# Performance work log

Hardware: AMD Instinct MI355X
Metric: run time of the kernel (lower is better)

Reference implementation:

```python
import jax, jax.numpy as jnp
import numpy as np

HIDDEN = 4096
N_HEADS = 32
N_KV = 32
HEAD_DIM = HIDDEN // N_HEADS  # 128
T = 2048
THETA = 10000.0
EPS = 1e-5


def setup_inputs() -> dict:
    key = jax.random.key(0)
    ks = jax.random.split(key, 7)
    s = 0.02
    return {
        "positions": jnp.arange(T, dtype=jnp.int64),
        "hidden_states": jax.random.normal(ks[0], (T, HIDDEN), jnp.float32),
        "w_qkv": jax.random.normal(ks[1], ((N_HEADS + 2 * N_KV) * HEAD_DIM, HIDDEN), jnp.float32) * s,
        "w_o": jax.random.normal(ks[2], (HIDDEN, N_HEADS * HEAD_DIM), jnp.float32) * s,
        "q_norm_w": jnp.ones((N_HEADS, HEAD_DIM), jnp.float32) + jax.random.normal(ks[3], (N_HEADS, HEAD_DIM), jnp.float32) * s,
        "q_norm_b": jax.random.normal(ks[4], (N_HEADS, HEAD_DIM), jnp.float32) * s,
        "k_norm_w": jnp.ones((N_KV, HEAD_DIM), jnp.float32) + jax.random.normal(ks[5], (N_KV, HEAD_DIM), jnp.float32) * s,
        "k_norm_b": jax.random.normal(ks[6], (N_KV, HEAD_DIM), jnp.float32) * s,
    }


def _layer_norm_affine(x, w, b):
    # x: [T, H, d]; normalize over last dim, no affine inside, then per-head affine
    mu = jnp.mean(x, axis=-1, keepdims=True)
    var = jnp.var(x, axis=-1, keepdims=True)
    xn = (x - mu) * jax.lax.rsqrt(var + EPS)
    return xn * w + b


def _rope_neox(x, positions):
    # x: [T, H, d], NEOX style: rotate halves over full head_dim
    half = HEAD_DIM // 2
    inv_freq = 1.0 / (THETA ** (jnp.arange(0, half, dtype=jnp.float32) * 2.0 / HEAD_DIM))
    ang = positions.astype(jnp.float32)[:, None] * inv_freq  # [T, half]
    cos = jnp.cos(ang)[:, None, :]
    sin = jnp.sin(ang)[:, None, :]
    x1, x2 = x[..., :half], x[..., half:]
    return jnp.concatenate([x1 * cos - x2 * sin, x2 * cos + x1 * sin], axis=-1)


def reference(positions, hidden_states, w_qkv, w_o, q_norm_w, q_norm_b, k_norm_w, k_norm_b):
    qkv = hidden_states @ w_qkv.T  # [T, (H+2Hkv)*d]
    q_size = N_HEADS * HEAD_DIM
    kv_size = N_KV * HEAD_DIM
    q = qkv[:, :q_size].reshape(T, N_HEADS, HEAD_DIM)
    k = qkv[:, q_size:q_size + kv_size].reshape(T, N_KV, HEAD_DIM)
    v = qkv[:, q_size + kv_size:].reshape(T, N_KV, HEAD_DIM)

    q = _layer_norm_affine(q, q_norm_w, q_norm_b)
    k = _layer_norm_affine(k, k_norm_w, k_norm_b)
    q = _rope_neox(q, positions)
    k = _rope_neox(k, positions)

    scale = HEAD_DIM ** -0.5
    scores = jnp.einsum('thd,shd->hts', q, k) * scale  # [H, T, T]
    causal = jnp.tril(jnp.ones((T, T), dtype=bool))
    scores = jnp.where(causal[None], scores, jnp.finfo(scores.dtype).min)
    p = jax.nn.softmax(scores, axis=-1)
    attn = jnp.einsum('hts,shd->thd', p, v).reshape(T, N_HEADS * HEAD_DIM)
    return attn @ w_o.T
```

## Files before the change

### kernel.cpp

```cpp
#include <hip/hip_runtime.h>
#include <cstdint>

#define T_SEQ 2048
#define HID   4096
#define NH    32
#define HD    128
#define QKVW  12288

typedef float  f32x4  __attribute__((ext_vector_type(4)));
typedef __bf16 bf16x8 __attribute__((ext_vector_type(8)));

#define QSCALE (0.08838834764831845f * 1.4426950408889634f)

__device__ __forceinline__ unsigned short f2bf(float f) {
  unsigned int u = __builtin_bit_cast(unsigned int, f);
  u += 0x7fffu + ((u >> 16) & 1u);
  return (unsigned short)(u >> 16);
}

__device__ __forceinline__ void gload_lds16(const void* gptr, void* lptr) {
  __builtin_amdgcn_global_load_lds(
      (const __attribute__((address_space(1))) unsigned int*)(unsigned long long)(uintptr_t)gptr,
      (__attribute__((address_space(3))) unsigned int*)(unsigned int)(uintptr_t)lptr,
      16, 0, 0);
}

#define SB __builtin_amdgcn_sched_barrier(0)

__global__ __launch_bounds__(256) void cast_bf16(const float* __restrict__ in,
                                                 unsigned short* __restrict__ out,
                                                 int n4) {
  int i = blockIdx.x * 256 + threadIdx.x;
  int stride = gridDim.x * 256;
  for (; i < n4; i += stride) {
    float4 v = ((const float4*)in)[i];
    ushort4 o;
    o.x = f2bf(v.x); o.y = f2bf(v.y); o.z = f2bf(v.z); o.w = f2bf(v.w);
    ((ushort4*)out)[i] = o;
  }
}

__global__ __launch_bounds__(512, 2) void gemm_bt(const unsigned short* __restrict__ Ag,
                                                  const unsigned short* __restrict__ Bg,
                                                  float* __restrict__ C,
                                                  int M, int N, int K, int MT) {
  __shared__ unsigned short As_[2][128 * 64];
  __shared__ unsigned short Bs_[2][256 * 64];
  const int tid  = threadIdx.x;
  const int lane = tid & 63;
  const int w    = tid >> 6;
  const int wm   = w >> 2;
  const int wn   = w & 3;
  const int l15  = lane & 15;
  const int lg   = lane >> 4;

  const int nwg = gridDim.x;
  const int cpx = nwg >> 3;
  const int swz = (blockIdx.x & 7) * cpx + (blockIdx.x >> 3);
  const int bm  = (swz % MT) * 128;
  const int bn  = (swz / MT) * 256;
  const int nk  = K >> 6;

#define STAGE_A(buf, kt_) do {                                                   \
    const unsigned short* _s = Ag + (size_t)bm * K + (size_t)(kt_) * 64;         \
    _Pragma("unroll")                                                            \
    for (int _u = 0; _u < 2; ++_u) {                                             \
      const int _cid = _u * 512 + tid;                                           \
      const int _r = _cid >> 3, _ch = _cid & 7;                                  \
      gload_lds16(_s + (size_t)_r * K + ((_ch ^ (_r & 7)) * 8),                  \
                  &As_[buf][(_u * 512 + w * 64) * 8]);                           \
    } } while (0)

#define STAGE_B(buf, kt_) do {                                                   \
    const unsigned short* _s = Bg + (size_t)bn * K + (size_t)(kt_) * 64;         \
    _Pragma("unroll")                                                            \
    for (int _u = 0; _u < 4; ++_u) {                                             \
      const int _cid = _u * 512 + tid;                                           \
      const int _r = _cid >> 3, _ch = _cid & 7;                                  \
      gload_lds16(_s + (size_t)_r * K + ((_ch ^ (_r & 7)) * 8),                  \
                  &Bs_[buf][(_u * 512 + w * 64) * 8]);                           \
    } } while (0)

  f32x4 acc[4][4] = {};

  STAGE_A(0, 0);
  STAGE_B(0, 0);
  if (nk > 1) {
    STAGE_B(1, 1);
    asm volatile("s_waitcnt vmcnt(4)" ::: "memory");
  } else {
    asm volatile("s_waitcnt vmcnt(0)" ::: "memory");
  }
  __builtin_amdgcn_s_barrier();

  for (int t = 0; t < nk; ++t) {
    const int cur = t & 1;
    bf16x8 bfr[4][2];
#pragma unroll
    for (int n = 0; n < 4; ++n)
#pragma unroll
      for (int kk = 0; kk < 2; ++kk) {
        const int r = wn * 64 + n * 16 + l15;
        bfr[n][kk] = *(const bf16x8*)&Bs_[cur][r * 64 + (((kk * 4 + lg) ^ (r & 7)) * 8)];
      }
    bf16x8 a0[2][2];
#pragma unroll
    for (int mi = 0; mi < 2; ++mi)
#pragma unroll
      for (int kk = 0; kk < 2; ++kk) {
        const int r = wm * 64 + mi * 16 + l15;
        a0[mi][kk] = *(const bf16x8*)&As_[cur][r * 64 + (((kk * 4 + lg) ^ (r & 7)) * 8)];
      }
    if (t + 1 < nk) STAGE_A(cur ^ 1, t + 1);
    __builtin_amdgcn_s_barrier();
    __builtin_amdgcn_s_setprio(1);
#pragma unroll
    for (int mi = 0; mi < 2; ++mi)
#pragma unroll
      for (int n = 0; n < 4; ++n)
#pragma unroll
        for (int kk = 0; kk < 2; ++kk)
          acc[mi][n] = __builtin_amdgcn_mfma_f32_16x16x32_bf16(a0[mi][kk], bfr[n][kk], acc[mi][n], 0, 0, 0);
    __builtin_amdgcn_s_setprio(0);
    __builtin_amdgcn_s_barrier();

    bf16x8 a1[2][2];
#pragma unroll
    for (int mi = 0; mi < 2; ++mi)
#pragma unroll
      for (int kk = 0; kk < 2; ++kk) {
        const int r = wm * 64 + (2 + mi) * 16 + l15;
        a1[mi][kk] = *(const bf16x8*)&As_[cur][r * 64 + (((kk * 4 + lg) ^ (r & 7)) * 8)];
      }
    if (t + 2 < nk) STAGE_B(cur, t + 2);
    __builtin_amdgcn_s_barrier();
    __builtin_amdgcn_s_setprio(1);
#pragma unroll
    for (int mi = 0; mi < 2; ++mi)
#pragma unroll
      for (int n = 0; n < 4; ++n)
#pragma unroll
        for (int kk = 0; kk < 2; ++kk)
          acc[2 + mi][n] = __builtin_amdgcn_mfma_f32_16x16x32_bf16(a1[mi][kk], bfr[n][kk], acc[2 + mi][n], 0, 0, 0);
    __builtin_amdgcn_s_setprio(0);
    if (t + 1 < nk) {
      if (t + 2 < nk) asm volatile("s_waitcnt vmcnt(4)" ::: "memory");
      else            asm volatile("s_waitcnt vmcnt(0)" ::: "memory");
      __builtin_amdgcn_sched_barrier(0);
    }
    __builtin_amdgcn_s_barrier();
  }
#undef STAGE_A
#undef STAGE_B

#pragma unroll
  for (int m = 0; m < 4; ++m)
#pragma unroll
    for (int i = 0; i < 4; ++i) {
      const int row = bm + wm * 64 + m * 16 + lg * 4 + i;
#pragma unroll
      for (int n = 0; n < 4; ++n)
        C[(size_t)row * N + bn + wn * 64 + n * 16 + l15] = acc[m][n][i];
    }
}

__global__ __launch_bounds__(512, 2) void gemm_bt8(const unsigned short* __restrict__ Ag,
                                                   const unsigned short* __restrict__ Bg,
                                                   float* __restrict__ C,
                                                   int M, int N, int K, int MT) {
  __shared__ unsigned short As_[2][256 * 64];
  __shared__ unsigned short Bs_[2][256 * 64];
  const int tid  = threadIdx.x;
  const int lane = tid & 63;
  const int w    = tid >> 6;
  const int wm   = w >> 2;
  const int wn   = w & 3;
  const int l15  = lane & 15;
  const int lg   = lane >> 4;
  const int sw   = l15 & 7;

  const int cpx = gridDim.x >> 3;
  const int swz = (blockIdx.x & 7) * cpx + (blockIdx.x >> 3);
  const int bm  = (swz % MT) * 256;
  const int bn  = (swz / MT) * 256;
  const int nk  = K >> 6;

  const unsigned short* Abase = Ag + (size_t)bm * K;
  const unsigned short* Bbase = Bg + (size_t)bn * K;

#define SG(ldsbase, gbase, kt_, u_) do {                                        \
    const int _cid = (u_) * 512 + tid;                                          \
    const int _r = _cid >> 3, _ch = _cid & 7;                                   \
    gload_lds16((gbase) + (size_t)_r * K + (size_t)(kt_) * 64 +                 \
                    ((_ch ^ (_r & 7)) * 8),                                     \
                (void*)((char*)(ldsbase) + _cid * 16));                         \
  } while (0)

#define RD(base, r, kk)                                                          \
  (*(const bf16x8*)((const char*)(base) + (r) * 128 + ((((kk) * 4 + lg) ^ sw) * 16)))

#define MFMA16(mbase, afr, bfr) do {                                             \
    _Pragma("unroll")                                                            \
    for (int _m = 0; _m < 4; ++_m)                                               \
      _Pragma("unroll")                                                          \
      for (int _n = 0; _n < 4; ++_n)                                             \
        acc[(mbase) + _m][_n] = __builtin_amdgcn_mfma_f32_16x16x32_bf16(         \
            afr[_m], bfr[_n], acc[(mbase) + _m][_n], 0, 0, 0);                   \
  } while (0)

  f32x4 acc[8][4] = {};

#pragma unroll
  for (int u = 0; u < 4; ++u) SG(As_[0], Abase, 0, u);
#pragma unroll
  for (int u = 0; u < 4; ++u) SG(Bs_[0], Bbase, 0, u);
  if (nk > 1) {
#pragma unroll
    for (int u = 0; u < 4; ++u) SG(As_[1], Abase, 1, u);
#pragma unroll
    for (int u = 0; u < 4; ++u) SG(Bs_[1], Bbase, 1, u);
    asm volatile("s_waitcnt vmcnt(8)" ::: "memory");
  } else {
    asm volatile("s_waitcnt vmcnt(0)" ::: "memory");
  }
  SB;
  __builtin_amdgcn_s_barrier();

  for (int t = 0; t < nk; ++t) {
    const int cur = t & 1;
    const unsigned short* As = As_[cur];
    const unsigned short* Bs = Bs_[cur];
    bf16x8 a0[4], a1[4], a2[4], a3[4], b0[4], b1[4];

#pragma unroll
    for (int m = 0; m < 4; ++m) a0[m] = RD(As, wm * 128 + m * 16 + l15, 0);
#pragma unroll
    for (int n = 0; n < 4; ++n) b0[n] = RD(Bs, wn * 64 + n * 16 + l15, 0);
    SB;
#pragma unroll
    for (int m = 0; m < 4; ++m) a1[m] = RD(As, wm * 128 + m * 16 + l15, 1);
#pragma unroll
    for (int n = 0; n < 4; ++n) b1[n] = RD(Bs, wn * 64 + n * 16 + l15, 1);
    SB;
    asm volatile("s_waitcnt lgkmcnt(8)" ::: "memory");
    SB;
    __builtin_amdgcn_s_setprio(1);
    MFMA16(0, a0, b0);
    __builtin_amdgcn_s_setprio(0);
#pragma unroll
    for (int m = 0; m < 4; ++m) a2[m] = RD(As, wm * 128 + (4 + m) * 16 + l15, 0);
    SB;
    asm volatile("s_waitcnt lgkmcnt(4)" ::: "memory");
    SB;
    __builtin_amdgcn_s_setprio(1);
    MFMA16(0, a1, b1);
    __builtin_amdgcn_s_setprio(0);
    __builtin_amdgcn_s_barrier();
#pragma unroll
    for (int m = 0; m < 4; ++m) a3[m] = RD(As, wm * 128 + (4 + m) * 16 + l15, 1);
    SB;
    if (t + 2 < nk) {
#pragma unroll
      for (int u = 0; u < 4; ++u) SG(As_[cur], Abase, t + 2, u);
#pragma unroll
      for (int u = 0; u < 4; ++u) SG(Bs_[cur], Bbase, t + 2, u);
    }
    SB;
    asm volatile("s_waitcnt lgkmcnt(4)" ::: "memory");
    SB;
    __builtin_amdgcn_s_setprio(1);
    MFMA16(4, a2, b0);
    __builtin_amdgcn_s_setprio(0);
    SB;
    asm volatile("s_waitcnt lgkmcnt(0)" ::: "memory");
    SB;
    __builtin_amdgcn_s_setprio(1);
    MFMA16(4, a3, b1);
    __builtin_amdgcn_s_setprio(0);
    if (t + 1 < nk) {
      if (t + 2 < nk) asm volatile("s_waitcnt vmcnt(8)" ::: "memory");
      else            asm volatile("s_waitcnt vmcnt(0)" ::: "memory");
      SB;
      __builtin_amdgcn_s_barrier();
    }
  }
#undef SG
#undef RD
#undef MFMA16

#pragma unroll
  for (int m = 0; m < 8; ++m)
#pragma unroll
    for (int i = 0; i < 4; ++i) {
      const int row = bm + wm * 128 + m * 16 + lg * 4 + i;
#pragma unroll
      for (int n = 0; n < 4; ++n)
        C[(size_t)row * N + bn + wn * 64 + n * 16 + l15] = acc[m][n][i];
    }
}

__global__ __launch_bounds__(256) void norm_rope(const float* __restrict__ qkv,
                                                 const float* __restrict__ qw,
                                                 const float* __restrict__ qb,
                                                 const float* __restrict__ kw,
                                                 const float* __restrict__ kb,
                                                 unsigned short* __restrict__ q,
                                                 unsigned short* __restrict__ k,
                                                 unsigned short* __restrict__ v) {
  const int t    = blockIdx.x;
  const int tid  = threadIdx.x;
  const int lane = tid & 63;
  const int w    = tid >> 6;
  const float invf = exp2f(-(float)lane * (13.287712379549449f / 64.0f));
  const float ang  = (float)t * invf;
  const float c = cosf(ang), s = sinf(ang);
  const float* row = qkv + (size_t)t * QKVW;

#pragma unroll 1
  for (int sel = 0; sel < 2; ++sel) {
    const float* src = row + sel * HID;
    const float* wgt = sel ? kw : qw;
    const float* bia = sel ? kb : qb;
    unsigned short* dst = sel ? k : q;
    const float oscale = sel ? 1.0f : QSCALE;
    for (int h = w; h < NH; h += 4) {
      const float* x = src + h * HD;
      float x1 = x[lane], x2 = x[lane + 64];
      float sum = x1 + x2, ss = x1 * x1 + x2 * x2;
#pragma unroll
      for (int m = 1; m < 64; m <<= 1) {
        sum += __shfl_xor(sum, m, 64);
        ss  += __shfl_xor(ss, m, 64);
      }
      const float mu  = sum * (1.0f / 128.0f);
      const float var = ss * (1.0f / 128.0f) - mu * mu;
      const float r   = rsqrtf(var + 1e-5f);
      const float n1  = (x1 - mu) * r * wgt[h * HD + lane]      + bia[h * HD + lane];
      const float n2  = (x2 - mu) * r * wgt[h * HD + lane + 64] + bia[h * HD + lane + 64];
      const float o1  = (n1 * c - n2 * s) * oscale;
      const float o2  = (n2 * c + n1 * s) * oscale;
      dst[(size_t)t * HID + h * HD + lane]      = f2bf(o1);
      dst[(size_t)t * HID + h * HD + lane + 64] = f2bf(o2);
    }
  }
  const float* vx = row + 2 * HID;
  unsigned short* vdst = v + (size_t)t * HID;
  for (int j = tid; j < HID / 4; j += 256) {
    float4 val = ((const float4*)vx)[j];
    ushort4 o;
    o.x = f2bf(val.x); o.y = f2bf(val.y); o.z = f2bf(val.z); o.w = f2bf(val.w);
    ((ushort4*)vdst)[j] = o;
  }
}

__global__ __launch_bounds__(256) void transpose_v(const unsigned short* __restrict__ v,
                                                   unsigned short* __restrict__ vt) {
  __shared__ unsigned short tile[64][65];
  const int h  = blockIdx.z;
  const int tt = blockIdx.x * 64;
  const int dd = blockIdx.y * 64;
  const int tid = threadIdx.x;
#pragma unroll
  for (int p = 0; p < 4; ++p) {
    int idx = p * 256 + tid;
    int r = idx >> 4, c4 = idx & 15;
    ushort4 val = *(const ushort4*)&v[(size_t)(tt + r) * HID + h * HD + dd + c4 * 4];
    tile[r][c4 * 4 + 0] = val.x;
    tile[r][c4 * 4 + 1] = val.y;
    tile[r][c4 * 4 + 2] = val.z;
    tile[r][c4 * 4 + 3] = val.w;
  }
  __syncthreads();
#pragma unroll
  for (int p = 0; p < 4; ++p) {
    int idx = p * 256 + tid;
    int r = idx >> 4, c4 = idx & 15;
    ushort4 o;
    o.x = tile[c4 * 4 + 0][r];
    o.y = tile[c4 * 4 + 1][r];
    o.z = tile[c4 * 4 + 2][r];
    o.w = tile[c4 * 4 + 3][r];
    *(ushort4*)&vt[((size_t)h * HD + dd + r) * T_SEQ + tt + c4 * 4] = o;
  }
}

__global__ __launch_bounds__(256) void attn_fwd(const unsigned short* __restrict__ Q,
                                                const unsigned short* __restrict__ K,
                                                const unsigned short* __restrict__ VT,
                                                unsigned short* __restrict__ O) {
  __shared__ unsigned short Ks[2][64 * 128];
  __shared__ unsigned short Vs[2][128 * 64];
  __shared__ unsigned short Ps[4][16 * 64];
  const int h    = blockIdx.y;
  const int pair = blockIdx.x;
  const int tid  = threadIdx.x;
  const int lane = tid & 63;
  const int w    = tid >> 6;
  const int l15  = lane & 15;
  const int lg   = lane >> 4;
  const int sw   = l15 & 7;

#pragma unroll 1
  for (int half = 0; half < 2; ++half) {
    const int qt   = half ? (31 - pair) : pair;
    const int qrow = qt * 64 + w * 16;

    bf16x8 qf[4];
#pragma unroll
    for (int kk = 0; kk < 4; ++kk)
      qf[kk] = *(const bf16x8*)&Q[(size_t)(qrow + l15) * HID + h * HD + kk * 32 + lg * 8];

    f32x4 o[8] = {};
    float mrow[4], lrow[4];
#pragma unroll
    for (int i = 0; i < 4; ++i) { mrow[i] = -1e30f; lrow[i] = 0.0f; }

    const int nkt = qt + 1;

    {
#pragma unroll
      for (int p = 0; p < 4; ++p) {
        const int c  = p * 256 + tid;
        const int kr = c >> 4, kc = c & 15;
        gload_lds16(&K[(size_t)kr * HID + h * HD + ((kc ^ (kr & 7)) * 8)],
                    &Ks[0][(p * 256 + w * 64) * 8]);
        const int vr = c >> 3, vc = c & 7;
        gload_lds16(&VT[((size_t)h * HD + vr) * T_SEQ + ((vc ^ (vr & 7)) * 8)],
                    &Vs[0][(p * 256 + w * 64) * 8]);
      }
    }
    __syncthreads();

#pragma unroll 1
    for (int kt = 0; kt < nkt; ++kt) {
      const int cur = kt & 1;
      if (kt + 1 < nkt) {
        const int k0 = (kt + 1) * 64;
#pragma unroll
        for (int p = 0; p < 4; ++p) {
          const int c  = p * 256 + tid;
          const int kr = c >> 4, kc = c & 15;
          gload_lds16(&K[(size_t)(k0 + kr) * HID + h * HD + ((kc ^ (kr & 7)) * 8)],
                      &Ks[cur ^ 1][(p * 256 + w * 64) * 8]);
          const int vr = c >> 3, vc = c & 7;
          gload_lds16(&VT[((size_t)h * HD + vr) * T_SEQ + k0 + ((vc ^ (vr & 7)) * 8)],
                      &Vs[cur ^ 1][(p * 256 + w * 64) * 8]);
        }
      }
      const unsigned short* ksb = Ks[cur];
      const unsigned short* vsb = Vs[cur];

      f32x4 sfr[4] = {};
#pragma unroll
      for (int n = 0; n < 4; ++n)
#pragma unroll
        for (int kk = 0; kk < 4; ++kk) {
          bf16x8 kf = *(const bf16x8*)&ksb[(n * 16 + l15) * 128 + ((kk * 4 + lg) ^ sw) * 8];
          sfr[n] = __builtin_amdgcn_mfma_f32_16x16x32_bf16(qf[kk], kf, sfr[n], 0, 0, 0);
        }

      if (kt == qt) {
#pragma unroll
        for (int n = 0; n < 4; ++n)
#pragma unroll
          for (int i = 0; i < 4; ++i)
            if (n * 16 + l15 > w * 16 + lg * 4 + i) sfr[n][i] = -1e30f;
      }

      float escale[4];
#pragma unroll
      for (int i = 0; i < 4; ++i) {
        float mx = fmaxf(fmaxf(sfr[0][i], sfr[1][i]), fmaxf(sfr[2][i], sfr[3][i]));
        mx = fmaxf(mx, __shfl_xor(mx, 1, 64));
        mx = fmaxf(mx, __shfl_xor(mx, 2, 64));
        mx = fmaxf(mx, __shfl_xor(mx, 4, 64));
        mx = fmaxf(mx, __shfl_xor(mx, 8, 64));
        const float mnew = fmaxf(mrow[i], mx);
        escale[i] = exp2f(mrow[i] - mnew);
        mrow[i] = mnew;
        const int prow = lg * 4 + i;
        float rs = 0.0f;
#pragma unroll
        for (int n = 0; n < 4; ++n) {
          const float p = exp2f(sfr[n][i] - mnew);
          rs += p;
          Ps[w][prow * 64 + (((2 * n + (l15 >> 3)) ^ (prow & 7)) * 8) + sw] = f2bf(p);
        }
        rs += __shfl_xor(rs, 1, 64);
        rs += __shfl_xor(rs, 2, 64);
        rs += __shfl_xor(rs, 4, 64);
        rs += __shfl_xor(rs, 8, 64);
        lrow[i] = lrow[i] * escale[i] + rs;
      }
#pragma unroll
      for (int f = 0; f < 8; ++f)
#pragma unroll
        for (int i = 0; i < 4; ++i) o[f][i] *= escale[i];

      asm volatile("s_waitcnt lgkmcnt(0)" ::: "memory");
      __builtin_amdgcn_sched_barrier(0);

      bf16x8 pf[2];
#pragma unroll
      for (int kk = 0; kk < 2; ++kk)
        pf[kk] = *(const bf16x8*)&Ps[w][l15 * 64 + ((kk * 4 + lg) ^ sw) * 8];
#pragma unroll
      for (int f = 0; f < 8; ++f)
#pragma unroll
        for (int kk = 0; kk < 2; ++kk) {
          bf16x8 vf = *(const bf16x8*)&vsb[(f * 16 + l15) * 64 + ((kk * 4 + lg) ^ sw) * 8];
          o[f] = __builtin_amdgcn_mfma_f32_16x16x32_bf16(pf[kk], vf, o[f], 0, 0, 0);
        }

      __syncthreads();
    }

#pragma unroll
    for (int i = 0; i < 4; ++i) {
      const float inv = 1.0f / lrow[i];
      const int trow = qrow + lg * 4 + i;
#pragma unroll
      for (int f = 0; f < 8; ++f)
        O[(size_t)trow * HID + h * HD + f * 16 + l15] = f2bf(o[f][i] * inv);
    }
  }
}

extern "C" void kernel_launch(void* const* d_in, const int* in_sizes, int n_in,
                              void* d_out, int out_size, void* d_ws, size_t ws_size,
                              hipStream_t stream) {
  const float* hidden = (const float*)d_in[1];
  const float* w_qkv  = (const float*)d_in[2];
  const float* w_o    = (const float*)d_in[3];
  const float* qw     = (const float*)d_in[4];
  const float* qb     = (const float*)d_in[5];
  const float* kw     = (const float*)d_in[6];
  const float* kb     = (const float*)d_in[7];

  char* ws = (char*)d_ws;
  unsigned short* wqkv_bf = (unsigned short*)(ws + 0);
  unsigned short* attn_bf = (unsigned short*)(ws + 0);
  unsigned short* wo_bf   = (unsigned short*)(ws + 16777216);
  unsigned short* hid_bf  = (unsigned short*)(ws + 100663296);
  unsigned short* vt_bf   = (unsigned short*)(ws + 100663296);
  float* qkv_f32          = (float*)(ws + 117440512);
  unsigned short* q_bf    = (unsigned short*)(ws + 218103808);
  unsigned short* k_bf    = (unsigned short*)(ws + 234881024);
  unsigned short* v_bf    = (unsigned short*)(ws + 251658240);

  cast_bf16<<<2048, 256, 0, stream>>>(hidden, hid_bf, (T_SEQ * HID) / 4);
  cast_bf16<<<2048, 256, 0, stream>>>(w_qkv, wqkv_bf, (QKVW * HID) / 4);
  gemm_bt8<<<384, 512, 0, stream>>>(hid_bf, wqkv_bf, qkv_f32, T_SEQ, QKVW, HID, 8);
  cast_bf16<<<2048, 256, 0, stream>>>(w_o, wo_bf, (HID * HID) / 4);
  norm_rope<<<T_SEQ, 256, 0, stream>>>(qkv_f32, qw, qb, kw, kb, q_bf, k_bf, v_bf);
  transpose_v<<<dim3(T_SEQ / 64, HD / 64, NH), 256, 0, stream>>>(v_bf, vt_bf);
  attn_fwd<<<dim3(16, NH), 256, 0, stream>>>(q_bf, k_bf, vt_bf, attn_bf);
  gemm_bt<<<256, 512, 0, stream>>>(attn_bf, wo_bf, (float*)d_out, T_SEQ, HID, HID, 16);
}
```

Baseline: 503.2 us.

## Emit bf16 QKV from GEMM, retile to 256x192, drop V cast pass

The QKV GEMM now writes bf16 output instead of fp32, which halves the intermediate write and read traffic. Its block tile moves from 256x256 to 256x192, giving a 512-block grid instead of 384 so the work spreads more evenly across CUs. norm_rope reads bf16 input and no longer copies V, and transpose_v reads V directly from the QKV buffer with stride QKVW. Rounding Q and K to bf16 before layer norm adds precision loss, and the narrower N tile lowers MFMA reuse per LDS load.

```diff
diff --git a/kernel.cpp b/kernel.cpp
--- a/kernel.cpp
+++ b/kernel.cpp
@@ -16,6 +16,9 @@
   unsigned int u = __builtin_bit_cast(unsigned int, f);
   u += 0x7fffu + ((u >> 16) & 1u);
   return (unsigned short)(u >> 16);
+}
+__device__ __forceinline__ float bf2f(unsigned short u) {
+  return __builtin_bit_cast(float, (unsigned int)u << 16);
 }
 
 __device__ __forceinline__ void gload_lds16(const void* gptr, void* lptr) {
@@ -166,10 +169,10 @@
 
 __global__ __launch_bounds__(512, 2) void gemm_bt8(const unsigned short* __restrict__ Ag,
                                                    const unsigned short* __restrict__ Bg,
-                                                   float* __restrict__ C,
+                                                   unsigned short* __restrict__ C,
                                                    int M, int N, int K, int MT) {
   __shared__ unsigned short As_[2][256 * 64];
-  __shared__ unsigned short Bs_[2][256 * 64];
+  __shared__ unsigned short Bs_[2][192 * 64];
   const int tid  = threadIdx.x;
   const int lane = tid & 63;
   const int w    = tid >> 6;
@@ -182,7 +185,7 @@
   const int cpx = gridDim.x >> 3;
   const int swz = (blockIdx.x & 7) * cpx + (blockIdx.x >> 3);
   const int bm  = (swz % MT) * 256;
-  const int bn  = (swz / MT) * 256;
+  const int bn  = (swz / MT) * 192;
   const int nk  = K >> 6;
 
   const unsigned short* Abase = Ag + (size_t)bm * K;
@@ -195,31 +198,31 @@
                     ((_ch ^ (_r & 7)) * 8),                                     \
                 (void*)((char*)(ldsbase) + _cid * 16));                         \
   } while (0)
+#define STAGE(abuf, bbuf, kt_) do {                                             \
+    SG(abuf, Abase, kt_, 0); SG(abuf, Abase, kt_, 1);                           \
+    SG(abuf, Abase, kt_, 2); SG(abuf, Abase, kt_, 3);                           \
+    SG(bbuf, Bbase, kt_, 0); SG(bbuf, Bbase, kt_, 1);                           \
+    SG(bbuf, Bbase, kt_, 2);                                                    \
+  } while (0)
 
 #define RD(base, r, kk)                                                          \
   (*(const bf16x8*)((const char*)(base) + (r) * 128 + ((((kk) * 4 + lg) ^ sw) * 16)))
 
-#define MFMA16(mbase, afr, bfr) do {                                             \
+#define MFMA12(mbase, afr, bfr) do {                                             \
     _Pragma("unroll")                                                            \
     for (int _m = 0; _m < 4; ++_m)                                               \
       _Pragma("unroll")                                                          \
-      for (int _n = 0; _n < 4; ++_n)                                             \
+      for (int _n = 0; _n < 3; ++_n)                                             \
         acc[(mbase) + _m][_n] = __builtin_amdgcn_mfma_f32_16x16x32_bf16(         \
             afr[_m], bfr[_n], acc[(mbase) + _m][_n], 0, 0, 0);                   \
   } while (0)
 
-  f32x4 acc[8][4] = {};
-
-#pragma unroll
-  for (int u = 0; u < 4; ++u) SG(As_[0], Abase, 0, u);
-#pragma unroll
-  for (int u = 0; u < 4; ++u) SG(Bs_[0], Bbase, 0, u);
+  f32x4 acc[8][3] = {};
+
+  STAGE(As_[0], Bs_[0], 0);
   if (nk > 1) {
-#pragma unroll
-    for (int u = 0; u < 4; ++u) SG(As_[1], Abase, 1, u);
-#pragma unroll
-    for (int u = 0; u < 4; ++u) SG(Bs_[1], Bbase, 1, u);
-    asm volatile("s_waitcnt vmcnt(8)" ::: "memory");
+    STAGE(As_[1], Bs_[1], 1);
+    asm volatile("s_waitcnt vmcnt(7)" ::: "memory");
   } else {
     asm volatile("s_waitcnt vmcnt(0)" ::: "memory");
   }
@@ -230,22 +233,22 @@
     const int cur = t & 1;
     const unsigned short* As = As_[cur];
     const unsigned short* Bs = Bs_[cur];
-    bf16x8 a0[4], a1[4], a2[4], a3[4], b0[4], b1[4];
+    bf16x8 a0[4], a1[4], a2[4], a3[4], b0[3], b1[3];
 
 #pragma unroll
     for (int m = 0; m < 4; ++m) a0[m] = RD(As, wm * 128 + m * 16 + l15, 0);
 #pragma unroll
-    for (int n = 0; n < 4; ++n) b0[n] = RD(Bs, wn * 64 + n * 16 + l15, 0);
+    for (int n = 0; n < 3; ++n) b0[n] = RD(Bs, wn * 48 + n * 16 + l15, 0);
     SB;
 #pragma unroll
     for (int m = 0; m < 4; ++m) a1[m] = RD(As, wm * 128 + m * 16 + l15, 1);
 #pragma unroll
-    for (int n = 0; n < 4; ++n) b1[n] = RD(Bs, wn * 64 + n * 16 + l15, 1);
-    SB;
-    asm volatile("s_waitcnt lgkmcnt(8)" ::: "memory");
+    for (int n = 0; n < 3; ++n) b1[n] = RD(Bs, wn * 48 + n * 16 + l15, 1);
+    SB;
+    asm volatile("s_waitcnt lgkmcnt(7)" ::: "memory");
     SB;
     __builtin_amdgcn_s_setprio(1);
-    MFMA16(0, a0, b0);
+    MFMA12(0, a0, b0);
     __builtin_amdgcn_s_setprio(0);
 #pragma unroll
     for (int m = 0; m < 4; ++m) a2[m] = RD(As, wm * 128 + (4 + m) * 16 + l15, 0);
@@ -253,40 +256,36 @@
     asm volatile("s_waitcnt lgkmcnt(4)" ::: "memory");
     SB;
     __builtin_amdgcn_s_setprio(1);
-    MFMA16(0, a1, b1);
+    MFMA12(0, a1, b1);
     __builtin_amdgcn_s_setprio(0);
+#pragma unroll
+    for (int m = 0; m < 4; ++m) a3[m] = RD(As, wm * 128 + (4 + m) * 16 + l15, 1);
+    SB;
     __builtin_amdgcn_s_barrier();
-#pragma unroll
-    for (int m = 0; m < 4; ++m) a3[m] = RD(As, wm * 128 + (4 + m) * 16 + l15, 1);
-    SB;
-    if (t + 2 < nk) {
-#pragma unroll
-      for (int u = 0; u < 4; ++u) SG(As_[cur], Abase, t + 2, u);
-#pragma unroll
-      for (int u = 0; u < 4; ++u) SG(Bs_[cur], Bbase, t + 2, u);
-    }
+    if (t + 2 < nk) STAGE(As_[cur], Bs_[cur], t + 2);
     SB;
     asm volatile("s_waitcnt lgkmcnt(4)" ::: "memory");
     SB;
     __builtin_amdgcn_s_setprio(1);
-    MFMA16(4, a2, b0);
+    MFMA12(4, a2, b0);
     __builtin_amdgcn_s_setprio(0);
     SB;
     asm volatile("s_waitcnt lgkmcnt(0)" ::: "memory");
     SB;
     __builtin_amdgcn_s_setprio(1);
-    MFMA16(4, a3, b1);
+    MFMA12(4, a3, b1);
     __builtin_amdgcn_s_setprio(0);
     if (t + 1 < nk) {
-      if (t + 2 < nk) asm volatile("s_waitcnt vmcnt(8)" ::: "memory");
+      if (t + 2 < nk) asm volatile("s_waitcnt vmcnt(7)" ::: "memory");
       else            asm volatile("s_waitcnt vmcnt(0)" ::: "memory");
       SB;
       __builtin_amdgcn_s_barrier();
     }
   }
 #undef SG
+#undef STAGE
 #undef RD
-#undef MFMA16
+#undef MFMA12
 
 #pragma unroll
   for (int m = 0; m < 8; ++m)
@@ -294,19 +293,18 @@
     for (int i = 0; i < 4; ++i) {
       const int row = bm + wm * 128 + m * 16 + lg * 4 + i;
 #pragma unroll
-      for (int n = 0; n < 4; ++n)
-        C[(size_t)row * N + bn + wn * 64 + n * 16 + l15] = acc[m][n][i];
-    }
-}
-
-__global__ __launch_bounds__(256) void norm_rope(const float* __restrict__ qkv,
+      for (int n = 0; n < 3; ++n)
+        C[(size_t)row * N + bn + wn * 48 + n * 16 + l15] = f2bf(acc[m][n][i]);
+    }
+}
+
+__global__ __launch_bounds__(256) void norm_rope(const unsigned short* __restrict__ qkv,
                                                  const float* __restrict__ qw,
                                                  const float* __restrict__ qb,
                                                  const float* __restrict__ kw,
                                                  const float* __restrict__ kb,
                                                  unsigned short* __restrict__ q,
-                                                 unsigned short* __restrict__ k,
-                                                 unsigned short* __restrict__ v) {
+                                                 unsigned short* __restrict__ k) {
   const int t    = blockIdx.x;
   const int tid  = threadIdx.x;
   const int lane = tid & 63;
@@ -314,18 +312,18 @@
   const float invf = exp2f(-(float)lane * (13.287712379549449f / 64.0f));
   const float ang  = (float)t * invf;
   const float c = cosf(ang), s = sinf(ang);
-  const float* row = qkv + (size_t)t * QKVW;
+  const unsigned short* row = qkv + (size_t)t * QKVW;
 
 #pragma unroll 1
   for (int sel = 0; sel < 2; ++sel) {
-    const float* src = row + sel * HID;
+    const unsigned short* src = row + sel * HID;
     const float* wgt = sel ? kw : qw;
     const float* bia = sel ? kb : qb;
     unsigned short* dst = sel ? k : q;
     const float oscale = sel ? 1.0f : QSCALE;
     for (int h = w; h < NH; h += 4) {
-      const float* x = src + h * HD;
-      float x1 = x[lane], x2 = x[lane + 64];
+      const unsigned short* x = src + h * HD;
+      float x1 = bf2f(x[lane]), x2 = bf2f(x[lane + 64]);
       float sum = x1 + x2, ss = x1 * x1 + x2 * x2;
 #pragma unroll
       for (int m = 1; m < 64; m <<= 1) {
@@ -343,14 +341,6 @@
       dst[(size_t)t * HID + h * HD + lane + 64] = f2bf(o2);
     }
   }
-  const float* vx = row + 2 * HID;
-  unsigned short* vdst = v + (size_t)t * HID;
-  for (int j = tid; j < HID / 4; j += 256) {
-    float4 val = ((const float4*)vx)[j];
-    ushort4 o;
-    o.x = f2bf(val.x); o.y = f2bf(val.y); o.z = f2bf(val.z); o.w = f2bf(val.w);
-    ((ushort4*)vdst)[j] = o;
-  }
 }
 
 __global__ __launch_bounds__(256) void transpose_v(const unsigned short* __restrict__ v,
@@ -364,7 +354,7 @@
   for (int p = 0; p < 4; ++p) {
     int idx = p * 256 + tid;
     int r = idx >> 4, c4 = idx & 15;
-    ushort4 val = *(const ushort4*)&v[(size_t)(tt + r) * HID + h * HD + dd + c4 * 4];
+    ushort4 val = *(const ushort4*)&v[(size_t)(tt + r) * QKVW + h * HD + dd + c4 * 4];
     tile[r][c4 * 4 + 0] = val.x;
     tile[r][c4 * 4 + 1] = val.y;
     tile[r][c4 * 4 + 2] = val.z;
@@ -543,17 +533,16 @@
   unsigned short* wo_bf   = (unsigned short*)(ws + 16777216);
   unsigned short* hid_bf  = (unsigned short*)(ws + 100663296);
   unsigned short* vt_bf   = (unsigned short*)(ws + 100663296);
-  float* qkv_f32          = (float*)(ws + 117440512);
-  unsigned short* q_bf    = (unsigned short*)(ws + 218103808);
-  unsigned short* k_bf    = (unsigned short*)(ws + 234881024);
-  unsigned short* v_bf    = (unsigned short*)(ws + 251658240);
+  unsigned short* qkv_bf  = (unsigned short*)(ws + 117440512);
+  unsigned short* q_bf    = (unsigned short*)(ws + 167772160);
+  unsigned short* k_bf    = (unsigned short*)(ws + 184549376);
 
   cast_bf16<<<2048, 256, 0, stream>>>(hidden, hid_bf, (T_SEQ * HID) / 4);
   cast_bf16<<<2048, 256, 0, stream>>>(w_qkv, wqkv_bf, (QKVW * HID) / 4);
-  gemm_bt8<<<384, 512, 0, stream>>>(hid_bf, wqkv_bf, qkv_f32, T_SEQ, QKVW, HID, 8);
+  gemm_bt8<<<512, 512, 0, stream>>>(hid_bf, wqkv_bf, qkv_bf, T_SEQ, QKVW, HID, 8);
   cast_bf16<<<2048, 256, 0, stream>>>(w_o, wo_bf, (HID * HID) / 4);
-  norm_rope<<<T_SEQ, 256, 0, stream>>>(qkv_f32, qw, qb, kw, kb, q_bf, k_bf, v_bf);
-  transpose_v<<<dim3(T_SEQ / 64, HD / 64, NH), 256, 0, stream>>>(v_bf, vt_bf);
+  norm_rope<<<T_SEQ, 256, 0, stream>>>(qkv_bf, qw, qb, kw, kb, q_bf, k_bf);
+  transpose_v<<<dim3(T_SEQ / 64, HD / 64, NH), 256, 0, stream>>>(qkv_bf + 2 * HID, vt_bf);
   attn_fwd<<<dim3(16, NH), 256, 0, stream>>>(q_bf, k_bf, vt_bf, attn_bf);
   gemm_bt<<<256, 512, 0, stream>>>(attn_bf, wo_bf, (float*)d_out, T_SEQ, HID, HID, 16);
 }
```

Result: faster. 462.3 us (-8.1%).
